# Optimization experiments

Hardware: AMD Instinct MI355X
Metric: run time of the kernel (lower is better)

Reference implementation:

```python
import jax, jax.numpy as jnp
import numpy as np

B, C_IN, N = 16, 64, 40962          # icosphere level-6 node count
C_OUT = 32                           # out_feats; conv emits 7*C_OUT channels
NEW_N = 4 * N - 6                    # 163842
SEVEN_N = 7 * N                      # gather domain after reshape


def setup_inputs() -> dict:
    key = jax.random.key(0)
    k1, k2, k3, k4, k5 = jax.random.split(key, 5)
    x = jax.random.normal(k1, (B, C_IN, N), dtype=jnp.float32)
    W = jax.random.normal(k2, (7 * C_OUT, C_IN), dtype=jnp.float32) * (1.0 / np.sqrt(C_IN))
    b = jax.random.normal(k3, (7 * C_OUT,), dtype=jnp.float32) * 0.01
    top_idx = jax.random.randint(k4, (N,), 0, SEVEN_N, dtype=jnp.int64 if jax.config.jax_enable_x64 else jnp.int32)
    down_idx = jax.random.randint(k5, ((3 * N - 6) * 2,), 0, SEVEN_N, dtype=jnp.int64 if jax.config.jax_enable_x64 else jnp.int32)
    return {"x": x, "W": W, "b": b, "top_idx": top_idx, "down_idx": down_idx}


def reference(x, W, b, top_idx, down_idx):
    Bsz, _, n = x.shape
    c_out = W.shape[0] // 7
    # pointwise (kernel_size=1) Conv1d == GEMM over channels: [B,7*out,N]
    y = jnp.einsum('bcn,oc->bon', x, W) + b[None, :, None]
    # torch .view(B, out, 7N): row-major reshape, identical in jax
    y = y.reshape(Bsz, c_out, 7 * n)
    x1 = y[:, :, top_idx]                               # [B, out, N]
    x2 = y[:, :, down_idx].reshape(Bsz, c_out, -1, 2)   # [B, out, 3N-6, 2]
    out = jnp.concatenate([x1, x2.mean(axis=3)], axis=2)  # [B, out, 4N-6]
    return out
```

## Files before the change

kernel.cpp:

```cpp
#include <hip/hip_runtime.h>
#include <hip/hip_fp16.h>

#define BB     16
#define CIN    64
#define NN     40962
#define COUT   32
#define NEWN   (4*NN - 6)
#define GROUPS_PER_B ((NEWN + 31)/32)
#define NGROUPS (BB * GROUPS_PER_B)

typedef _Float16 f16x8  __attribute__((ext_vector_type(8)));
typedef float    f32x16 __attribute__((ext_vector_type(16)));
typedef _Float16 h2     __attribute__((ext_vector_type(2)));

__device__ __forceinline__ int pk_add_h2(int a, int b) {
  h2 r = __builtin_bit_cast(h2, a) + __builtin_bit_cast(h2, b);
  return __builtin_bit_cast(int, r);
}
__device__ __forceinline__ int pack2(float lo, float hi) {
  h2 r; r.x = (_Float16)lo; r.y = (_Float16)hi;
  return __builtin_bit_cast(int, r);
}

__global__ __launch_bounds__(256) void k_transpose(const float* __restrict__ x,
                                                   __half* __restrict__ xT) {
  __shared__ float tile[64][65];
  const int b   = blockIdx.y;
  const int n0  = blockIdx.x * 64;
  const int tid = threadIdx.x;
  const float* xb = x + (size_t)b * CIN * NN;

  const int cr8 = tid >> 5;
  const int nh  = tid & 31;
  if (n0 + 64 <= NN) {
#pragma unroll
    for (int p = 0; p < 8; ++p) {
      const int c = p * 8 + cr8;
      float2 v = *reinterpret_cast<const float2*>(xb + (size_t)c * NN + n0 + nh * 2);
      tile[c][nh * 2 + 0] = v.x;
      tile[c][nh * 2 + 1] = v.y;
    }
  } else {
#pragma unroll
    for (int p = 0; p < 8; ++p) {
      const int c = p * 8 + cr8;
      const int na = n0 + nh * 2, nb = na + 1;
      tile[c][nh * 2 + 0] = (na < NN) ? xb[(size_t)c * NN + na] : 0.f;
      tile[c][nh * 2 + 1] = (nb < NN) ? xb[(size_t)c * NN + nb] : 0.f;
    }
  }
  __syncthreads();

  __half* xTb = xT + (size_t)b * NN * CIN;
  const int nr = tid >> 3;
  const int ch = tid & 7;
#pragma unroll
  for (int p = 0; p < 2; ++p) {
    const int nl = p * 32 + nr;
    const int n  = n0 + nl;
    if (n < NN) {
      int4 v;
      v.x = pack2(tile[ch * 8 + 0][nl], tile[ch * 8 + 1][nl]);
      v.y = pack2(tile[ch * 8 + 2][nl], tile[ch * 8 + 3][nl]);
      v.z = pack2(tile[ch * 8 + 4][nl], tile[ch * 8 + 5][nl]);
      v.w = pack2(tile[ch * 8 + 6][nl], tile[ch * 8 + 7][nl]);
      *reinterpret_cast<int4*>(xTb + (size_t)n * CIN + ch * 8) = v;
    }
  }
}

struct GD {
  int4 c0[4], c1[4];
  int  t0, t1;
  int  b, k;
  bool valid;
};

__device__ __forceinline__ GD load_group(int gid, const __half* __restrict__ xT,
                                         const int* __restrict__ top,
                                         const int* __restrict__ down,
                                         int co, int h) {
  GD d;
  const int b = gid / GROUPS_PER_B;
  const int g = gid - b * GROUPS_PER_B;
  const int k = g * 32 + co;
  d.b = b; d.k = k;
  d.valid = (k < NEWN);
  int j1 = 0, j2 = 0;
  if (d.valid) {
    if (k < NN) { j1 = top[k]; j2 = j1; }
    else {
      int2 jj = *reinterpret_cast<const int2*>(down + 2 * (k - NN));
      j1 = jj.x; j2 = jj.y;
    }
  }
  const int t0 = j1 / NN, n0 = j1 - t0 * NN;
  const int t1 = j2 / NN, n1 = j2 - t1 * NN;
  d.t0 = t0; d.t1 = t1;
  const __half* xTb = xT + (size_t)b * NN * CIN;
  const int4* b0 = (const int4*)(xTb + (size_t)n0 * CIN);
  const int4* b1 = (const int4*)(xTb + (size_t)n1 * CIN);
#pragma unroll
  for (int q = 0; q < 4; ++q) d.c0[q] = b0[2 * q + h];
#pragma unroll
  for (int q = 0; q < 4; ++q) d.c1[q] = b1[2 * q + h];
  return d;
}

__device__ __forceinline__ void compute_store(const GD& d, const int4* __restrict__ Af,
                                              float* __restrict__ out, int h) {
  f32x16 acc;
#pragma unroll
  for (int i = 0; i < 16; ++i) acc[i] = 0.f;
  const int t0 = d.t0, t1 = d.t1;

#pragma unroll
  for (int s = 0; s < 28; ++s) {
    const int t = s >> 2, q = s & 3;
    const bool m0 = (t0 == t), m1 = (t1 == t);
    int4 bb;
    bb.x = pk_add_h2(m0 ? d.c0[q].x : 0, m1 ? d.c1[q].x : 0);
    bb.y = pk_add_h2(m0 ? d.c0[q].y : 0, m1 ? d.c1[q].y : 0);
    bb.z = pk_add_h2(m0 ? d.c0[q].z : 0, m1 ? d.c1[q].z : 0);
    bb.w = pk_add_h2(m0 ? d.c0[q].w : 0, m1 ? d.c1[q].w : 0);
    acc = __builtin_amdgcn_mfma_f32_32x32x16_f16(
        __builtin_bit_cast(f16x8, Af[s]), __builtin_bit_cast(f16x8, bb), acc, 0, 0, 0);
  }

  {
    int4 bsel = {0, 0, 0, 0};
    if (h == 0) {
      bsel.x = pack2((float)((t0 == 0) + (t1 == 0)), (float)((t0 == 1) + (t1 == 1)));
      bsel.y = pack2((float)((t0 == 2) + (t1 == 2)), (float)((t0 == 3) + (t1 == 3)));
      bsel.z = pack2((float)((t0 == 4) + (t1 == 4)), (float)((t0 == 5) + (t1 == 5)));
      bsel.w = pack2((float)((t0 == 6) + (t1 == 6)), 0.f);
    }
    acc = __builtin_amdgcn_mfma_f32_32x32x16_f16(
        __builtin_bit_cast(f16x8, Af[28]), __builtin_bit_cast(f16x8, bsel), acc, 0, 0, 0);
  }

  if (d.valid) {
    float* ob = out + (size_t)d.b * COUT * NEWN + d.k;
#pragma unroll
    for (int r = 0; r < 16; ++r) {
      const int corow = (r & 3) + 8 * (r >> 2) + 4 * h;
      __builtin_nontemporal_store(acc[r], ob + (size_t)corow * NEWN);
    }
  }
}

__global__ __launch_bounds__(256, 2) void k_upconv_mfma(
    const __half* __restrict__ xT, const float* __restrict__ W,
    const float* __restrict__ bias, const int* __restrict__ top,
    const int* __restrict__ down, float* __restrict__ out) {
  const int lane = threadIdx.x & 63;
  const int co   = lane & 31;
  const int h    = lane >> 5;
  const int gwave  = blockIdx.x * (blockDim.x >> 6) + (threadIdx.x >> 6);
  const int nwaves = gridDim.x * (blockDim.x >> 6);

  int4 Af[29];
#pragma unroll
  for (int s = 0; s < 28; ++s) {
    const int t  = s >> 2;
    const int c0 = 16 * (s & 3) + 8 * h;
    const float* wr = W + (co * 7 + t) * 64 + c0;
    float4 wa = *(const float4*)wr;
    float4 wb = *(const float4*)(wr + 4);
    Af[s].x = pack2(0.5f * wa.x, 0.5f * wa.y);
    Af[s].y = pack2(0.5f * wa.z, 0.5f * wa.w);
    Af[s].z = pack2(0.5f * wb.x, 0.5f * wb.y);
    Af[s].w = pack2(0.5f * wb.z, 0.5f * wb.w);
  }
  {
    int4 ab = {0, 0, 0, 0};
    if (h == 0) {
      float bv[8];
#pragma unroll
      for (int tau = 0; tau < 7; ++tau) bv[tau] = 0.5f * bias[co * 7 + tau];
      bv[7] = 0.f;
      ab.x = pack2(bv[0], bv[1]);
      ab.y = pack2(bv[2], bv[3]);
      ab.z = pack2(bv[4], bv[5]);
      ab.w = pack2(bv[6], bv[7]);
    }
    Af[28] = ab;
  }

  int gid = gwave;
  GD a = load_group(gid, xT, top, down, co, h);
  for (;;) {
    const int g1 = gid + nwaves;
    const bool h1 = (g1 < NGROUPS);
    GD bN;
    if (h1) bN = load_group(g1, xT, top, down, co, h);
    compute_store(a, Af, out, h);
    if (!h1) return;

    const int g2 = g1 + nwaves;
    const bool h2 = (g2 < NGROUPS);
    if (h2) a = load_group(g2, xT, top, down, co, h);
    compute_store(bN, Af, out, h);
    if (!h2) return;
    gid = g2;
  }
}

#define WPB 68
#define TPB (32*WPB + 4)

__global__ __launch_bounds__(256) void k_upconv_f32(
    const float* __restrict__ x, const float* __restrict__ W,
    const float* __restrict__ bias, const int* __restrict__ top,
    const int* __restrict__ down, float* __restrict__ out) {
  __shared__ float wl[7 * TPB];
  __shared__ float bl[224];
  const int tid = threadIdx.x;
  for (int p = tid; p < 224 * 64; p += 256) {
    int o = p >> 6, c = p & 63;
    wl[(o % 7) * TPB + (o / 7) * WPB + c] = W[p];
  }
  if (tid < 224) bl[tid] = bias[tid];
  __syncthreads();

  const int b = blockIdx.y;
  const int k = blockIdx.x * 256 + tid;

  int nit = 0, t0 = 0, t1 = 0, n0 = 0, n1 = 0;
  if (k < NEWN) {
    if (k < NN) {
      int j = top[k];
      t0 = j / NN; n0 = j - t0 * NN; nit = 1;
    } else {
      int kk = k - NN;
      int j1 = down[2 * kk], j2 = down[2 * kk + 1];
      t0 = j1 / NN; n0 = j1 - t0 * NN;
      t1 = j2 / NN; n1 = j2 - t1 * NN;
      nit = 2;
    }
  }

  float acc[32];
#pragma unroll
  for (int i = 0; i < 32; ++i) acc[i] = 0.f;

  for (int it = 0; it < nit; ++it) {
    const int t = it ? t1 : t0;
    const int n = it ? n1 : n0;
    const float* col = x + (size_t)b * CIN * NN + n;
    const int base = t * TPB;
#pragma unroll
    for (int ch = 0; ch < 8; ++ch) {
      float xv[8];
#pragma unroll
      for (int q = 0; q < 8; ++q) xv[q] = col[(size_t)(ch * 8 + q) * NN];
#pragma unroll
      for (int co = 0; co < 32; ++co) {
        float a = acc[co];
        const float* wr = &wl[base + co * WPB + ch * 8];
        float4 w0 = *(const float4*)(wr);
        float4 w1 = *(const float4*)(wr + 4);
        a += w0.x * xv[0]; a += w0.y * xv[1]; a += w0.z * xv[2]; a += w0.w * xv[3];
        a += w1.x * xv[4]; a += w1.y * xv[5]; a += w1.z * xv[6]; a += w1.w * xv[7];
        acc[co] = a;
      }
    }
  }

  if (k < NEWN) {
    float* ob = out + (size_t)b * COUT * NEWN + k;
    if (k < NN) {
#pragma unroll
      for (int co = 0; co < 32; ++co)
        ob[(size_t)co * NEWN] = acc[co] + bl[co * 7 + t0];
    } else {
#pragma unroll
      for (int co = 0; co < 32; ++co)
        ob[(size_t)co * NEWN] = 0.5f * (acc[co] + bl[co * 7 + t0] + bl[co * 7 + t1]);
    }
  }
}

extern "C" void kernel_launch(void* const* d_in, const int* in_sizes, int n_in,
                              void* d_out, int out_size, void* d_ws, size_t ws_size,
                              hipStream_t stream) {
  const float* x    = (const float*)d_in[0];
  const float* W    = (const float*)d_in[1];
  const float* bias = (const float*)d_in[2];
  const int*   top  = (const int*)d_in[3];
  const int*   down = (const int*)d_in[4];
  float* out = (float*)d_out;

  const size_t xT_bytes = (size_t)BB * NN * CIN * sizeof(__half);
  if (ws_size >= xT_bytes) {
    __half* xT = (__half*)d_ws;
    k_transpose<<<dim3((NN + 63) / 64, BB), 256, 0, stream>>>(x, xT);
    k_upconv_mfma<<<dim3(512), 256, 0, stream>>>(xT, W, bias, top, down, out);
  } else {
    k_upconv_f32<<<dim3((NEWN + 255) / 256, BB), 256, 0, stream>>>(x, W, bias, top, down, out);
  }
}
```

Baseline: 673.4 us.

## Move MFMA weight fragments to LDS and raise occupancy with more blocks

Weight/bias A-fragments now live in shared memory (29x64 int4) instead of 29 int4 registers per lane. Occupancy rises from 2 to 4 blocks per CU and the grid grows from 512 to 2048. The explicit two-stage software prefetch is replaced by a simple grid-stride loop that relies on occupancy to hide gather latency. Block IDs are swizzled across XCDs, and a fast path for the pure-top groups skips the second gather. Costs are an LDS read per MFMA step, the loss of manual prefetch overlap, and per-block weight setup repeated across four times as many blocks.

```diff
diff --git a/kernel.cpp b/kernel.cpp
--- a/kernel.cpp
+++ b/kernel.cpp
@@ -69,140 +69,131 @@
   }
 }
 
-struct GD {
-  int4 c0[4], c1[4];
-  int  t0, t1;
-  int  b, k;
-  bool valid;
-};
-
-__device__ __forceinline__ GD load_group(int gid, const __half* __restrict__ xT,
-                                         const int* __restrict__ top,
-                                         const int* __restrict__ down,
-                                         int co, int h) {
-  GD d;
-  const int b = gid / GROUPS_PER_B;
-  const int g = gid - b * GROUPS_PER_B;
-  const int k = g * 32 + co;
-  d.b = b; d.k = k;
-  d.valid = (k < NEWN);
-  int j1 = 0, j2 = 0;
-  if (d.valid) {
-    if (k < NN) { j1 = top[k]; j2 = j1; }
-    else {
-      int2 jj = *reinterpret_cast<const int2*>(down + 2 * (k - NN));
-      j1 = jj.x; j2 = jj.y;
-    }
-  }
-  const int t0 = j1 / NN, n0 = j1 - t0 * NN;
-  const int t1 = j2 / NN, n1 = j2 - t1 * NN;
-  d.t0 = t0; d.t1 = t1;
-  const __half* xTb = xT + (size_t)b * NN * CIN;
-  const int4* b0 = (const int4*)(xTb + (size_t)n0 * CIN);
-  const int4* b1 = (const int4*)(xTb + (size_t)n1 * CIN);
-#pragma unroll
-  for (int q = 0; q < 4; ++q) d.c0[q] = b0[2 * q + h];
-#pragma unroll
-  for (int q = 0; q < 4; ++q) d.c1[q] = b1[2 * q + h];
-  return d;
-}
-
-__device__ __forceinline__ void compute_store(const GD& d, const int4* __restrict__ Af,
-                                              float* __restrict__ out, int h) {
-  f32x16 acc;
-#pragma unroll
-  for (int i = 0; i < 16; ++i) acc[i] = 0.f;
-  const int t0 = d.t0, t1 = d.t1;
-
-#pragma unroll
-  for (int s = 0; s < 28; ++s) {
-    const int t = s >> 2, q = s & 3;
-    const bool m0 = (t0 == t), m1 = (t1 == t);
-    int4 bb;
-    bb.x = pk_add_h2(m0 ? d.c0[q].x : 0, m1 ? d.c1[q].x : 0);
-    bb.y = pk_add_h2(m0 ? d.c0[q].y : 0, m1 ? d.c1[q].y : 0);
-    bb.z = pk_add_h2(m0 ? d.c0[q].z : 0, m1 ? d.c1[q].z : 0);
-    bb.w = pk_add_h2(m0 ? d.c0[q].w : 0, m1 ? d.c1[q].w : 0);
-    acc = __builtin_amdgcn_mfma_f32_32x32x16_f16(
-        __builtin_bit_cast(f16x8, Af[s]), __builtin_bit_cast(f16x8, bb), acc, 0, 0, 0);
-  }
-
-  {
-    int4 bsel = {0, 0, 0, 0};
-    if (h == 0) {
-      bsel.x = pack2((float)((t0 == 0) + (t1 == 0)), (float)((t0 == 1) + (t1 == 1)));
-      bsel.y = pack2((float)((t0 == 2) + (t1 == 2)), (float)((t0 == 3) + (t1 == 3)));
-      bsel.z = pack2((float)((t0 == 4) + (t1 == 4)), (float)((t0 == 5) + (t1 == 5)));
-      bsel.w = pack2((float)((t0 == 6) + (t1 == 6)), 0.f);
-    }
-    acc = __builtin_amdgcn_mfma_f32_32x32x16_f16(
-        __builtin_bit_cast(f16x8, Af[28]), __builtin_bit_cast(f16x8, bsel), acc, 0, 0, 0);
-  }
-
-  if (d.valid) {
-    float* ob = out + (size_t)d.b * COUT * NEWN + d.k;
-#pragma unroll
-    for (int r = 0; r < 16; ++r) {
-      const int corow = (r & 3) + 8 * (r >> 2) + 4 * h;
-      __builtin_nontemporal_store(acc[r], ob + (size_t)corow * NEWN);
-    }
-  }
-}
-
-__global__ __launch_bounds__(256, 2) void k_upconv_mfma(
+__global__ __launch_bounds__(256, 4) void k_upconv_mfma(
     const __half* __restrict__ xT, const float* __restrict__ W,
     const float* __restrict__ bias, const int* __restrict__ top,
     const int* __restrict__ down, float* __restrict__ out) {
-  const int lane = threadIdx.x & 63;
+  __shared__ int4 Aflds[29][64];
+  const int tid  = threadIdx.x;
+  const int lane = tid & 63;
   const int co   = lane & 31;
   const int h    = lane >> 5;
-  const int gwave  = blockIdx.x * (blockDim.x >> 6) + (threadIdx.x >> 6);
-  const int nwaves = gridDim.x * (blockDim.x >> 6);
-
-  int4 Af[29];
-#pragma unroll
-  for (int s = 0; s < 28; ++s) {
+
+  for (int p = tid; p < 28 * 64; p += 256) {
+    const int s  = p >> 6, l = p & 63;
+    const int lc = l & 31, lh = l >> 5;
     const int t  = s >> 2;
-    const int c0 = 16 * (s & 3) + 8 * h;
-    const float* wr = W + (co * 7 + t) * 64 + c0;
+    const int c0 = 16 * (s & 3) + 8 * lh;
+    const float* wr = W + (lc * 7 + t) * 64 + c0;
     float4 wa = *(const float4*)wr;
     float4 wb = *(const float4*)(wr + 4);
-    Af[s].x = pack2(0.5f * wa.x, 0.5f * wa.y);
-    Af[s].y = pack2(0.5f * wa.z, 0.5f * wa.w);
-    Af[s].z = pack2(0.5f * wb.x, 0.5f * wb.y);
-    Af[s].w = pack2(0.5f * wb.z, 0.5f * wb.w);
-  }
-  {
+    int4 v;
+    v.x = pack2(0.5f * wa.x, 0.5f * wa.y);
+    v.y = pack2(0.5f * wa.z, 0.5f * wa.w);
+    v.z = pack2(0.5f * wb.x, 0.5f * wb.y);
+    v.w = pack2(0.5f * wb.z, 0.5f * wb.w);
+    Aflds[s][l] = v;
+  }
+  if (tid < 64) {
     int4 ab = {0, 0, 0, 0};
-    if (h == 0) {
+    if ((tid >> 5) == 0) {
+      const int lc = tid & 31;
       float bv[8];
 #pragma unroll
-      for (int tau = 0; tau < 7; ++tau) bv[tau] = 0.5f * bias[co * 7 + tau];
+      for (int tau = 0; tau < 7; ++tau) bv[tau] = 0.5f * bias[lc * 7 + tau];
       bv[7] = 0.f;
       ab.x = pack2(bv[0], bv[1]);
       ab.y = pack2(bv[2], bv[3]);
       ab.z = pack2(bv[4], bv[5]);
       ab.w = pack2(bv[6], bv[7]);
     }
-    Af[28] = ab;
-  }
-
-  int gid = gwave;
-  GD a = load_group(gid, xT, top, down, co, h);
-  for (;;) {
-    const int g1 = gid + nwaves;
-    const bool h1 = (g1 < NGROUPS);
-    GD bN;
-    if (h1) bN = load_group(g1, xT, top, down, co, h);
-    compute_store(a, Af, out, h);
-    if (!h1) return;
-
-    const int g2 = g1 + nwaves;
-    const bool h2 = (g2 < NGROUPS);
-    if (h2) a = load_group(g2, xT, top, down, co, h);
-    compute_store(bN, Af, out, h);
-    if (!h2) return;
-    gid = g2;
+    Aflds[28][tid] = ab;
+  }
+  __syncthreads();
+
+  const int nblocks = gridDim.x;
+  const int sbid = (blockIdx.x & 7) * (nblocks >> 3) + (blockIdx.x >> 3);
+  const int gwave  = sbid * (blockDim.x >> 6) + (tid >> 6);
+  const int nwaves = nblocks * (blockDim.x >> 6);
+
+  for (int gid = gwave; gid < NGROUPS; gid += nwaves) {
+    const int b = gid / GROUPS_PER_B;
+    const int g = gid - b * GROUPS_PER_B;
+    const int k = g * 32 + co;
+    const __half* xTb = xT + (size_t)b * NN * CIN;
+
+    int4 col0[4], col1[4];
+    int t0, t1;
+    bool valid = true;
+
+    if (g * 32 + 31 < NN) {
+      const int j1 = top[k];
+      t0 = j1 / NN; t1 = t0;
+      const int n0 = j1 - t0 * NN;
+      const int4* base0 = (const int4*)(xTb + (size_t)n0 * CIN);
+#pragma unroll
+      for (int q = 0; q < 4; ++q) col0[q] = base0[2 * q + h];
+#pragma unroll
+      for (int q = 0; q < 4; ++q) col1[q] = col0[q];
+    } else {
+      valid = (k < NEWN);
+      int j1 = 0, j2 = 0;
+      if (valid) {
+        if (k < NN) { j1 = top[k]; j2 = j1; }
+        else {
+          int2 jj = *reinterpret_cast<const int2*>(down + 2 * (k - NN));
+          j1 = jj.x; j2 = jj.y;
+        }
+      }
+      t0 = j1 / NN; const int n0 = j1 - t0 * NN;
+      t1 = j2 / NN; const int n1 = j2 - t1 * NN;
+      const int4* base0 = (const int4*)(xTb + (size_t)n0 * CIN);
+      const int4* base1 = (const int4*)(xTb + (size_t)n1 * CIN);
+#pragma unroll
+      for (int q = 0; q < 4; ++q) col0[q] = base0[2 * q + h];
+#pragma unroll
+      for (int q = 0; q < 4; ++q) col1[q] = base1[2 * q + h];
+    }
+
+    f32x16 acc;
+#pragma unroll
+    for (int i = 0; i < 16; ++i) acc[i] = 0.f;
+
+#pragma unroll
+    for (int s = 0; s < 28; ++s) {
+      const int t = s >> 2, q = s & 3;
+      const bool m0 = (t0 == t), m1 = (t1 == t);
+      int4 bb;
+      bb.x = pk_add_h2(m0 ? col0[q].x : 0, m1 ? col1[q].x : 0);
+      bb.y = pk_add_h2(m0 ? col0[q].y : 0, m1 ? col1[q].y : 0);
+      bb.z = pk_add_h2(m0 ? col0[q].z : 0, m1 ? col1[q].z : 0);
+      bb.w = pk_add_h2(m0 ? col0[q].w : 0, m1 ? col1[q].w : 0);
+      const int4 a_s = Aflds[s][lane];
+      acc = __builtin_amdgcn_mfma_f32_32x32x16_f16(
+          __builtin_bit_cast(f16x8, a_s), __builtin_bit_cast(f16x8, bb), acc, 0, 0, 0);
+    }
+
+    {
+      int4 bsel = {0, 0, 0, 0};
+      if (h == 0) {
+        bsel.x = pack2((float)((t0 == 0) + (t1 == 0)), (float)((t0 == 1) + (t1 == 1)));
+        bsel.y = pack2((float)((t0 == 2) + (t1 == 2)), (float)((t0 == 3) + (t1 == 3)));
+        bsel.z = pack2((float)((t0 == 4) + (t1 == 4)), (float)((t0 == 5) + (t1 == 5)));
+        bsel.w = pack2((float)((t0 == 6) + (t1 == 6)), 0.f);
+      }
+      const int4 a28 = Aflds[28][lane];
+      acc = __builtin_amdgcn_mfma_f32_32x32x16_f16(
+          __builtin_bit_cast(f16x8, a28), __builtin_bit_cast(f16x8, bsel), acc, 0, 0, 0);
+    }
+
+    if (valid) {
+      float* ob = out + (size_t)b * COUT * NEWN + k;
+#pragma unroll
+      for (int r = 0; r < 16; ++r) {
+        const int corow = (r & 3) + 8 * (r >> 2) + 4 * h;
+        __builtin_nontemporal_store(acc[r], ob + (size_t)corow * NEWN);
+      }
+    }
   }
 }
 
@@ -295,7 +286,7 @@
   if (ws_size >= xT_bytes) {
     __half* xT = (__half*)d_ws;
     k_transpose<<<dim3((NN + 63) / 64, BB), 256, 0, stream>>>(x, xT);
-    k_upconv_mfma<<<dim3(512), 256, 0, stream>>>(xT, W, bias, top, down, out);
+    k_upconv_mfma<<<dim3(2048), 256, 0, stream>>>(xT, W, bias, top, down, out);
   } else {
     k_upconv_f32<<<dim3((NEWN + 255) / 256, BB), 256, 0, stream>>>(x, W, bias, top, down, out);
   }
```

After: 735.0 us. 9.2% more time.
